# Optimization experiments

Measured on AMD Instinct MI355X. Metric: run time of the kernel, lower is better.

The kernel has to match this reference:

```python
import jax, jax.numpy as jnp
import numpy as np

N = 100000   # nodes
DEG = 4      # fixed out-degree (>2 so every node survives the c>2 mask)
E = N * DEG  # edges
IN = 128
H = 256


def _lin_params(key, fan_out, fan_in, bias=True):
    k1, k2 = jax.random.split(key)
    W = 0.05 * jax.random.normal(k1, (fan_out, fan_in), jnp.float32)
    if bias:
        b = 0.05 * jax.random.normal(k2, (fan_out,), jnp.float32)
        return W, b
    return W


def setup_inputs() -> dict:
    key = jax.random.key(0)
    ks = jax.random.split(key, 12)
    x = jax.random.normal(ks[0], (N, IN), jnp.float32)
    # every node has exactly DEG outgoing edges -> out-degree 4 > 2 for all nodes
    src = jnp.repeat(jnp.arange(N, dtype=jnp.int32), DEG)
    dst = jax.random.randint(ks[1], (E,), 0, N, dtype=jnp.int32)
    edge_index = jnp.stack([src, dst])  # [2, E]
    batch = jnp.zeros((N,), jnp.int32)
    Wr0, br0 = _lin_params(ks[2], H, IN)
    Ws0 = _lin_params(ks[3], H, IN, bias=False)
    Wr1, br1 = _lin_params(ks[4], H, H)
    Ws1 = _lin_params(ks[5], H, H, bias=False)
    Wr2, br2 = _lin_params(ks[6], H, H)
    Ws2 = _lin_params(ks[7], H, H, bias=False)
    Wsp1, bsp1 = _lin_params(ks[8], 1, H)
    Wsp2, bsp2 = _lin_params(ks[9], 1, H)
    Wl, bl = _lin_params(ks[10], 1, 2)
    return dict(x=x, edge_index=edge_index, batch=batch,
                Wr0=Wr0, br0=br0, Ws0=Ws0,
                Wr1=Wr1, br1=br1, Ws1=Ws1,
                Wr2=Wr2, br2=br2, Ws2=Ws2,
                Wsp1=Wsp1, bsp1=bsp1, Wsp2=Wsp2, bsp2=bsp2,
                Wl=Wl, bl=bl)


def reference(x, edge_index, batch, Wr0, br0, Ws0, Wr1, br1, Ws1,
              Wr2, br2, Ws2, Wsp1, bsp1, Wsp2, bsp2, Wl, bl):
    src, dst = edge_index[0], edge_index[1]

    def gconv(h, Wr, br, Ws):
        # PyG GraphConv(aggr='add'): out_i = W_rel @ sum_{j->i} h_j + b + W_root @ h_i
        agg = jax.ops.segment_sum(h[src], dst, num_segments=N)
        return jax.nn.relu(agg @ Wr.T + br + h @ Ws.T)

    h = gconv(x, Wr0, br0, Ws0)
    h = gconv(h, Wr1, br1, Ws1)
    h = gconv(h, Wr2, br2, Ws2)

    # unique(edge_index[0], counts) ; keep source nodes with out-degree > 2
    deg = jax.ops.segment_sum(jnp.ones((E,), h.dtype), src, num_segments=N)
    sel = jnp.nonzero(deg > 2, size=N, fill_value=0)[0]  # all N nodes by construction
    xs = h[sel].reshape(-1, 2 * H)  # pair consecutive nodes
    x1, x2 = xs[:, :H], xs[:, H:]
    out = jnp.concatenate([jax.nn.relu(x1 @ Wsp1.T + bsp1),
                           jax.nn.relu(x2 @ Wsp2.T + bsp2)], axis=1)
    y = jax.nn.sigmoid(out @ Wl.T + bl)  # split=True branch
    return y, xs, x1, x2
```

## Files before the change

### kernel.cpp

```cpp
#include <hip/hip_runtime.h>
#include <hip/hip_bf16.h>
#include <math.h>

#define NNODES 100000
#define NEDGES 400000
#define INDIM  128
#define HDIM   256
#define MAXDEG 32

#define BM 128
#define BN 128
#define BK 64
#define MTILES 782
#define GEMM_BLOCKS 1568

typedef __attribute__((ext_vector_type(8))) short short8;
typedef __attribute__((ext_vector_type(8))) unsigned short ushort8v;
typedef __attribute__((ext_vector_type(4))) float f32x4;

__device__ __forceinline__ float bf2f(unsigned short u) {
    union { unsigned int i; float f; } v; v.i = ((unsigned int)u) << 16; return v.f;
}
__device__ __forceinline__ unsigned short f2bf(float f) {
    union { float f; unsigned int i; } v; v.f = f;
    unsigned int r = v.i + 0x7fffu + ((v.i >> 16) & 1u);
    return (unsigned short)(r >> 16);
}

__device__ __forceinline__ void async_load16(const void* g, void* l) {
    __builtin_amdgcn_global_load_lds(
        (const __attribute__((address_space(1))) unsigned int*)g,
        (__attribute__((address_space(3))) unsigned int*)l,
        16, 0, 0);
}

__global__ void build_elist(const int* __restrict__ ei, int* __restrict__ cnt,
                            int* __restrict__ elist) {
    int e = blockIdx.x * 256 + threadIdx.x;
    if (e < NEDGES) {
        int d = ei[NEDGES + e];
        int s = ei[e];
        int pos = atomicAdd(&cnt[d], 1);
        if (pos < MAXDEG) elist[d * MAXDEG + pos] = s;
    }
}

__global__ void convert_x(const float* __restrict__ x, unsigned short* __restrict__ xb) {
    int i = blockIdx.x * 256 + threadIdx.x;
    const int total = NNODES * INDIM / 4;
    if (i < total) {
        float4 v = ((const float4*)x)[i];
        ushort4 o; o.x = f2bf(v.x); o.y = f2bf(v.y); o.z = f2bf(v.z); o.w = f2bf(v.w);
        ((ushort4*)xb)[i] = o;
    }
}

__global__ void convert_w(const float* __restrict__ Wr, const float* __restrict__ Ws,
                          unsigned short* __restrict__ B, int K) {
    int idx = blockIdx.x * 256 + threadIdx.x;
    int tot = HDIM * 2 * K;
    if (idx < tot) {
        int n = idx / (2 * K);
        int k = idx - n * 2 * K;
        float v = (k < K) ? Wr[n * K + k] : Ws[n * K + (k - K)];
        B[idx] = f2bf(v);
    }
}

__global__ void gather_f32(const float* __restrict__ x, const int* __restrict__ cnt,
                           const int* __restrict__ elist, unsigned short* __restrict__ agg) {
    int wid  = (blockIdx.x * blockDim.x + threadIdx.x) >> 6;
    int lane = threadIdx.x & 63;
    if (wid >= NNODES) return;
    int c = cnt[wid]; if (c > MAXDEG) c = MAXDEG;
    const int4* el4 = (const int4*)(elist + wid * MAXDEG);
    float a0 = 0.f, a1 = 0.f;
    for (int j0 = 0; j0 < c; j0 += 4) {
        int4 e = el4[j0 >> 2];
        int rem = c - j0;
        float2 v0 = {0.f,0.f}, v1 = {0.f,0.f}, v2 = {0.f,0.f}, v3 = {0.f,0.f};
        v0 = ((const float2*)(x + (size_t)e.x * INDIM))[lane];
        if (rem > 1) v1 = ((const float2*)(x + (size_t)e.y * INDIM))[lane];
        if (rem > 2) v2 = ((const float2*)(x + (size_t)e.z * INDIM))[lane];
        if (rem > 3) v3 = ((const float2*)(x + (size_t)e.w * INDIM))[lane];
        a0 += v0.x + v1.x + v2.x + v3.x;
        a1 += v0.y + v1.y + v2.y + v3.y;
    }
    ushort2 o; o.x = f2bf(a0); o.y = f2bf(a1);
    ((ushort2*)(agg + (size_t)wid * INDIM))[lane] = o;
}

__global__ void gather_bf16(const unsigned short* __restrict__ h, const int* __restrict__ cnt,
                            const int* __restrict__ elist, unsigned short* __restrict__ agg) {
    int wid  = (blockIdx.x * blockDim.x + threadIdx.x) >> 6;
    int lane = threadIdx.x & 63;
    if (wid >= NNODES) return;
    int c = cnt[wid]; if (c > MAXDEG) c = MAXDEG;
    const int4* el4 = (const int4*)(elist + wid * MAXDEG);
    float a0 = 0.f, a1 = 0.f, a2 = 0.f, a3 = 0.f;
    for (int j0 = 0; j0 < c; j0 += 4) {
        int4 e = el4[j0 >> 2];
        int rem = c - j0;
        ushort4 v0 = {0,0,0,0}, v1 = {0,0,0,0}, v2 = {0,0,0,0}, v3 = {0,0,0,0};
        v0 = ((const ushort4*)(h + (size_t)e.x * HDIM))[lane];
        if (rem > 1) v1 = ((const ushort4*)(h + (size_t)e.y * HDIM))[lane];
        if (rem > 2) v2 = ((const ushort4*)(h + (size_t)e.z * HDIM))[lane];
        if (rem > 3) v3 = ((const ushort4*)(h + (size_t)e.w * HDIM))[lane];
        a0 += bf2f(v0.x) + bf2f(v1.x) + bf2f(v2.x) + bf2f(v3.x);
        a1 += bf2f(v0.y) + bf2f(v1.y) + bf2f(v2.y) + bf2f(v3.y);
        a2 += bf2f(v0.z) + bf2f(v1.z) + bf2f(v2.z) + bf2f(v3.z);
        a3 += bf2f(v0.w) + bf2f(v1.w) + bf2f(v2.w) + bf2f(v3.w);
    }
    ushort4 o; o.x = f2bf(a0); o.y = f2bf(a1); o.z = f2bf(a2); o.w = f2bf(a3);
    ((ushort4*)(agg + (size_t)wid * HDIM))[lane] = o;
}

template<int MODE>
__global__ __launch_bounds__(256)
void gemm_kernel(const unsigned short* __restrict__ A1, const unsigned short* __restrict__ A2,
                 int K, const unsigned short* __restrict__ B, const float* __restrict__ bias,
                 unsigned short* __restrict__ hout,
                 float* __restrict__ xs, float* __restrict__ x1o, float* __restrict__ x2o,
                 const float* __restrict__ Wsp1, const float* __restrict__ Wsp2,
                 float* __restrict__ spart) {
    __shared__ __align__(16) unsigned char smem[(BM * BK + BN * BK) * 2];
    unsigned short* Ash = (unsigned short*)smem;
    unsigned short* Bsh = Ash + BM * BK;

    int u = blockIdx.x;
    int g = u >> 4, r = u & 15;
    int ny = (r >> 3) & 1;
    int mx = g * 8 + (r & 7);
    if (mx >= MTILES) return;

    const int tid  = threadIdx.x;
    const int lane = tid & 63;
    const int wave = tid >> 6;
    const int wm = wave >> 1, wn = wave & 1;
    const int m0 = mx * BM;
    const int n0 = ny * BN;
    const int Ktot = 2 * K;

    f32x4 acc[4][4];
    for (int i = 0; i < 4; i++)
        for (int j = 0; j < 4; j++)
            acc[i][j] = (f32x4){0.f, 0.f, 0.f, 0.f};

    for (int k0 = 0; k0 < Ktot; k0 += BK) {
        const unsigned short* Abase; int koff;
        if (k0 < K) { Abase = A1; koff = k0; } else { Abase = A2; koff = k0 - K; }

        #pragma unroll
        for (int it = 0; it < 4; it++) {
            int idx = it * 256 + tid;
            int row = idx >> 3, seg = idx & 7;
            int gseg = seg ^ (row & 7);
            int grow = m0 + row; if (grow >= NNODES) grow = NNODES - 1;
            async_load16(Abase + (size_t)grow * K + koff + gseg * 8, &Ash[idx * 8]);
        }
        #pragma unroll
        for (int it = 0; it < 4; it++) {
            int idx = it * 256 + tid;
            int row = idx >> 3, seg = idx & 7;
            int gseg = seg ^ (row & 7);
            int grow = n0 + row;
            async_load16(B + (size_t)grow * Ktot + k0 + gseg * 8, &Bsh[idx * 8]);
        }
        __syncthreads();

        #pragma unroll
        for (int half = 0; half < 2; half++) {
            short8 af[4], bfr[4];
            #pragma unroll
            for (int mt = 0; mt < 4; mt++) {
                int ml  = wm * 64 + mt * 16 + (lane & 15);
                int seg = half * 4 + (lane >> 4);
                int ps  = seg ^ (ml & 7);
                af[mt] = *(const short8*)&Ash[ml * BK + ps * 8];
            }
            #pragma unroll
            for (int nt = 0; nt < 4; nt++) {
                int nl  = wn * 64 + nt * 16 + (lane & 15);
                int seg = half * 4 + (lane >> 4);
                int ps  = seg ^ (nl & 7);
                bfr[nt] = *(const short8*)&Bsh[nl * BK + ps * 8];
            }
            #pragma unroll
            for (int mt = 0; mt < 4; mt++)
                #pragma unroll
                for (int nt = 0; nt < 4; nt++)
                    acc[mt][nt] = __builtin_amdgcn_mfma_f32_16x16x32_bf16(
                        af[mt], bfr[nt], acc[mt][nt], 0, 0, 0);
        }
        __syncthreads();
    }

    float* bounce = (float*)smem;
    float* wb = bounce + wave * (16 * 68);
    const int q    = lane & 3;
    const int rrow = lane >> 2;

    #pragma unroll
    for (int mt = 0; mt < 4; mt++) {
        __syncthreads();
        #pragma unroll
        for (int nt = 0; nt < 4; nt++)
            #pragma unroll
            for (int rr = 0; rr < 4; rr++)
                wb[((lane >> 4) * 4 + rr) * 68 + nt * 16 + (lane & 15)] = acc[mt][nt][rr];
        __syncthreads();

        int grow = m0 + wm * 64 + mt * 16 + rrow;
        int gc   = n0 + wn * 64 + q * 16;
        float4 v[4];
        #pragma unroll
        for (int s = 0; s < 4; s++)
            v[s] = ((const float4*)(wb + rrow * 68 + q * 16))[s];

        if (grow < NNODES) {
            const float4* bv = (const float4*)(bias + gc);
            #pragma unroll
            for (int s = 0; s < 4; s++) {
                float4 b4 = bv[s];
                v[s].x = fmaxf(v[s].x + b4.x, 0.f);
                v[s].y = fmaxf(v[s].y + b4.y, 0.f);
                v[s].z = fmaxf(v[s].z + b4.z, 0.f);
                v[s].w = fmaxf(v[s].w + b4.w, 0.f);
            }
            if (MODE == 0) {
                ushort8v o0, o1;
                o0[0]=f2bf(v[0].x); o0[1]=f2bf(v[0].y); o0[2]=f2bf(v[0].z); o0[3]=f2bf(v[0].w);
                o0[4]=f2bf(v[1].x); o0[5]=f2bf(v[1].y); o0[6]=f2bf(v[1].z); o0[7]=f2bf(v[1].w);
                o1[0]=f2bf(v[2].x); o1[1]=f2bf(v[2].y); o1[2]=f2bf(v[2].z); o1[3]=f2bf(v[2].w);
                o1[4]=f2bf(v[3].x); o1[5]=f2bf(v[3].y); o1[6]=f2bf(v[3].z); o1[7]=f2bf(v[3].w);
                ushort8v* dst = (ushort8v*)(hout + (size_t)grow * HDIM + gc);
                dst[0] = o0; dst[1] = o1;
            } else {
                float4* xsp = (float4*)(xs + (size_t)grow * HDIM + gc);
                #pragma unroll
                for (int s = 0; s < 4; s++) xsp[s] = v[s];
                float* xo = (grow & 1) ? x2o : x1o;
                float4* xop = (float4*)(xo + (size_t)(grow >> 1) * HDIM + gc);
                #pragma unroll
                for (int s = 0; s < 4; s++) xop[s] = v[s];
                const float* wsp = (grow & 1) ? Wsp2 : Wsp1;
                const float4* wv = (const float4*)(wsp + gc);
                float p = 0.f;
                #pragma unroll
                for (int s = 0; s < 4; s++) {
                    float4 w4 = wv[s];
                    p += v[s].x * w4.x + v[s].y * w4.y + v[s].z * w4.z + v[s].w * w4.w;
                }
                p += __shfl_xor(p, 1);
                p += __shfl_xor(p, 2);
                if (q == 0) atomicAdd(&spart[grow], p);
            }
        }
    }
}

__global__ void finalize_kernel(const float* __restrict__ spart, const float* __restrict__ bsp1,
                                const float* __restrict__ bsp2, const float* __restrict__ Wl,
                                const float* __restrict__ bl, float* __restrict__ y) {
    int p = blockIdx.x * 256 + threadIdx.x;
    if (p < NNODES / 2) {
        float s1 = spart[2 * p]     + bsp1[0]; s1 = s1 > 0.f ? s1 : 0.f;
        float s2 = spart[2 * p + 1] + bsp2[0]; s2 = s2 > 0.f ? s2 : 0.f;
        float t = s1 * Wl[0] + s2 * Wl[1] + bl[0];
        y[p] = 1.f / (1.f + expf(-t));
    }
}

extern "C" void kernel_launch(void* const* d_in, const int* in_sizes, int n_in,
                              void* d_out, int out_size, void* d_ws, size_t ws_size,
                              hipStream_t stream) {
    const float* x    = (const float*)d_in[0];
    const int*   ei   = (const int*)d_in[1];
    const float* Wr0  = (const float*)d_in[3];
    const float* br0  = (const float*)d_in[4];
    const float* Ws0  = (const float*)d_in[5];
    const float* Wr1  = (const float*)d_in[6];
    const float* br1  = (const float*)d_in[7];
    const float* Ws1  = (const float*)d_in[8];
    const float* Wr2  = (const float*)d_in[9];
    const float* br2  = (const float*)d_in[10];
    const float* Ws2  = (const float*)d_in[11];
    const float* Wsp1 = (const float*)d_in[12];
    const float* bsp1 = (const float*)d_in[13];
    const float* Wsp2 = (const float*)d_in[14];
    const float* bsp2 = (const float*)d_in[15];
    const float* Wl   = (const float*)d_in[16];
    const float* bl   = (const float*)d_in[17];

    char* ws = (char*)d_ws;
    size_t off = 0;
    auto alloc = [&](size_t bytes) -> void* {
        void* p = ws + off;
        off += (bytes + 255) & ~(size_t)255;
        return p;
    };
    int*            cnt   = (int*)alloc((size_t)NNODES * 4);
    float*          spart = (float*)alloc((size_t)NNODES * 4);
    size_t zero_bytes = off;
    int*            elist = (int*)alloc((size_t)NNODES * MAXDEG * 4);
    unsigned short* xb    = (unsigned short*)alloc((size_t)NNODES * INDIM * 2);
    unsigned short* aggb  = (unsigned short*)alloc((size_t)NNODES * HDIM * 2);
    unsigned short* hA    = (unsigned short*)alloc((size_t)NNODES * HDIM * 2);
    unsigned short* hB    = (unsigned short*)alloc((size_t)NNODES * HDIM * 2);
    unsigned short* B0    = (unsigned short*)alloc((size_t)HDIM * 2 * INDIM * 2);
    unsigned short* B1    = (unsigned short*)alloc((size_t)HDIM * 2 * HDIM * 2);
    unsigned short* B2    = (unsigned short*)alloc((size_t)HDIM * 2 * HDIM * 2);

    float* y  = (float*)d_out;
    float* xs = y + 50000;
    float* x1 = xs + (size_t)50000 * 512;
    float* x2 = x1 + (size_t)50000 * 256;

    hipMemsetAsync(ws, 0, zero_bytes, stream);
    build_elist<<<(NEDGES + 255) / 256, 256, 0, stream>>>(ei, cnt, elist);
    convert_x<<<(NNODES * INDIM / 4 + 255) / 256, 256, 0, stream>>>(x, xb);
    convert_w<<<(HDIM * 2 * INDIM + 255) / 256, 256, 0, stream>>>(Wr0, Ws0, B0, INDIM);
    convert_w<<<(HDIM * 2 * HDIM + 255) / 256, 256, 0, stream>>>(Wr1, Ws1, B1, HDIM);
    convert_w<<<(HDIM * 2 * HDIM + 255) / 256, 256, 0, stream>>>(Wr2, Ws2, B2, HDIM);

    int gather_blocks = (NNODES * 64 + 255) / 256;

    gather_f32<<<gather_blocks, 256, 0, stream>>>(x, cnt, elist, aggb);
    gemm_kernel<0><<<GEMM_BLOCKS, 256, 0, stream>>>(aggb, xb, INDIM, B0, br0, hA,
                                                    nullptr, nullptr, nullptr,
                                                    nullptr, nullptr, nullptr);
    gather_bf16<<<gather_blocks, 256, 0, stream>>>(hA, cnt, elist, aggb);
    gemm_kernel<0><<<GEMM_BLOCKS, 256, 0, stream>>>(aggb, hA, HDIM, B1, br1, hB,
                                                    nullptr, nullptr, nullptr,
                                                    nullptr, nullptr, nullptr);
    gather_bf16<<<gather_blocks, 256, 0, stream>>>(hB, cnt, elist, aggb);
    gemm_kernel<1><<<GEMM_BLOCKS, 256, 0, stream>>>(aggb, hB, HDIM, B2, br2, nullptr,
                                                    xs, x1, x2, Wsp1, Wsp2, spart);
    finalize_kernel<<<(NNODES / 2 + 255) / 256, 256, 0, stream>>>(
        spart, bsp1, bsp2, Wl, bl, y);
}
```

Measured before the change: 618.3 us.

## Use 64x256 GEMM tiles, fuse prep kernels, gather layer-0 from bf16 input

The GEMM tile changes from 128x128 to 64x256. Each block now covers the full output width, so the A rows are read only once, and the wave layout and block indexing are reworked to match. The four prep launches (x conversion, three weight conversions, edge-list build) are merged into one kernel. The first gather now reads the bf16 copy of x instead of fp32, halving the bytes it reads. The trade-off is that each block now loads a larger B tile and layer-0 aggregation sums bf16-rounded inputs.

```diff
diff --git a/kernel.cpp b/kernel.cpp
--- a/kernel.cpp
+++ b/kernel.cpp
@@ -8,11 +8,10 @@
 #define HDIM   256
 #define MAXDEG 32
 
-#define BM 128
-#define BN 128
+#define BM 64
+#define BN 256
 #define BK 64
-#define MTILES 782
-#define GEMM_BLOCKS 1568
+#define MTILES 1563
 
 typedef __attribute__((ext_vector_type(8))) short short8;
 typedef __attribute__((ext_vector_type(8))) unsigned short ushort8v;
@@ -34,9 +33,44 @@
         16, 0, 0);
 }
 
-__global__ void build_elist(const int* __restrict__ ei, int* __restrict__ cnt,
+#define XB_BLOCKS 12500
+#define W0_BLOCKS 256
+#define W1_BLOCKS 512
+#define EL_BLOCKS 1563
+#define PREP_BLOCKS (XB_BLOCKS + W0_BLOCKS + 2 * W1_BLOCKS + EL_BLOCKS)
+
+__global__ void prep_kernel(const float* __restrict__ x, unsigned short* __restrict__ xb,
+                            const float* __restrict__ Wr0, const float* __restrict__ Ws0,
+                            unsigned short* __restrict__ B0,
+                            const float* __restrict__ Wr1, const float* __restrict__ Ws1,
+                            unsigned short* __restrict__ B1,
+                            const float* __restrict__ Wr2, const float* __restrict__ Ws2,
+                            unsigned short* __restrict__ B2,
+                            const int* __restrict__ ei, int* __restrict__ cnt,
                             int* __restrict__ elist) {
-    int e = blockIdx.x * 256 + threadIdx.x;
+    int b = blockIdx.x;
+    if (b < XB_BLOCKS) {
+        int i = b * 256 + threadIdx.x;
+        float4 v = ((const float4*)x)[i];
+        ushort4 o; o.x = f2bf(v.x); o.y = f2bf(v.y); o.z = f2bf(v.z); o.w = f2bf(v.w);
+        ((ushort4*)xb)[i] = o;
+        return;
+    }
+    b -= XB_BLOCKS;
+    if (b < W0_BLOCKS + 2 * W1_BLOCKS) {
+        const float *Wr, *Ws; unsigned short* B; int K;
+        if (b < W0_BLOCKS)               { Wr = Wr0; Ws = Ws0; B = B0; K = INDIM; }
+        else if (b < W0_BLOCKS + W1_BLOCKS) { Wr = Wr1; Ws = Ws1; B = B1; K = HDIM; b -= W0_BLOCKS; }
+        else                              { Wr = Wr2; Ws = Ws2; B = B2; K = HDIM; b -= W0_BLOCKS + W1_BLOCKS; }
+        int idx = b * 256 + threadIdx.x;
+        int n = idx / (2 * K);
+        int k = idx - n * 2 * K;
+        float v = (k < K) ? Wr[n * K + k] : Ws[n * K + (k - K)];
+        B[idx] = f2bf(v);
+        return;
+    }
+    b -= W0_BLOCKS + 2 * W1_BLOCKS;
+    int e = b * 256 + threadIdx.x;
     if (e < NEDGES) {
         int d = ei[NEDGES + e];
         int s = ei[e];
@@ -45,30 +79,8 @@
     }
 }
 
-__global__ void convert_x(const float* __restrict__ x, unsigned short* __restrict__ xb) {
-    int i = blockIdx.x * 256 + threadIdx.x;
-    const int total = NNODES * INDIM / 4;
-    if (i < total) {
-        float4 v = ((const float4*)x)[i];
-        ushort4 o; o.x = f2bf(v.x); o.y = f2bf(v.y); o.z = f2bf(v.z); o.w = f2bf(v.w);
-        ((ushort4*)xb)[i] = o;
-    }
-}
-
-__global__ void convert_w(const float* __restrict__ Wr, const float* __restrict__ Ws,
-                          unsigned short* __restrict__ B, int K) {
-    int idx = blockIdx.x * 256 + threadIdx.x;
-    int tot = HDIM * 2 * K;
-    if (idx < tot) {
-        int n = idx / (2 * K);
-        int k = idx - n * 2 * K;
-        float v = (k < K) ? Wr[n * K + k] : Ws[n * K + (k - K)];
-        B[idx] = f2bf(v);
-    }
-}
-
-__global__ void gather_f32(const float* __restrict__ x, const int* __restrict__ cnt,
-                           const int* __restrict__ elist, unsigned short* __restrict__ agg) {
+__global__ void gather_bf16_128(const unsigned short* __restrict__ h, const int* __restrict__ cnt,
+                                const int* __restrict__ elist, unsigned short* __restrict__ agg) {
     int wid  = (blockIdx.x * blockDim.x + threadIdx.x) >> 6;
     int lane = threadIdx.x & 63;
     if (wid >= NNODES) return;
@@ -78,20 +90,20 @@
     for (int j0 = 0; j0 < c; j0 += 4) {
         int4 e = el4[j0 >> 2];
         int rem = c - j0;
-        float2 v0 = {0.f,0.f}, v1 = {0.f,0.f}, v2 = {0.f,0.f}, v3 = {0.f,0.f};
-        v0 = ((const float2*)(x + (size_t)e.x * INDIM))[lane];
-        if (rem > 1) v1 = ((const float2*)(x + (size_t)e.y * INDIM))[lane];
-        if (rem > 2) v2 = ((const float2*)(x + (size_t)e.z * INDIM))[lane];
-        if (rem > 3) v3 = ((const float2*)(x + (size_t)e.w * INDIM))[lane];
-        a0 += v0.x + v1.x + v2.x + v3.x;
-        a1 += v0.y + v1.y + v2.y + v3.y;
+        ushort2 v0 = {0,0}, v1 = {0,0}, v2 = {0,0}, v3 = {0,0};
+        v0 = ((const ushort2*)(h + (size_t)e.x * INDIM))[lane];
+        if (rem > 1) v1 = ((const ushort2*)(h + (size_t)e.y * INDIM))[lane];
+        if (rem > 2) v2 = ((const ushort2*)(h + (size_t)e.z * INDIM))[lane];
+        if (rem > 3) v3 = ((const ushort2*)(h + (size_t)e.w * INDIM))[lane];
+        a0 += bf2f(v0.x) + bf2f(v1.x) + bf2f(v2.x) + bf2f(v3.x);
+        a1 += bf2f(v0.y) + bf2f(v1.y) + bf2f(v2.y) + bf2f(v3.y);
     }
     ushort2 o; o.x = f2bf(a0); o.y = f2bf(a1);
     ((ushort2*)(agg + (size_t)wid * INDIM))[lane] = o;
 }
 
-__global__ void gather_bf16(const unsigned short* __restrict__ h, const int* __restrict__ cnt,
-                            const int* __restrict__ elist, unsigned short* __restrict__ agg) {
+__global__ void gather_bf16_256(const unsigned short* __restrict__ h, const int* __restrict__ cnt,
+                                const int* __restrict__ elist, unsigned short* __restrict__ agg) {
     int wid  = (blockIdx.x * blockDim.x + threadIdx.x) >> 6;
     int lane = threadIdx.x & 63;
     if (wid >= NNODES) return;
@@ -127,18 +139,10 @@
     unsigned short* Ash = (unsigned short*)smem;
     unsigned short* Bsh = Ash + BM * BK;
 
-    int u = blockIdx.x;
-    int g = u >> 4, r = u & 15;
-    int ny = (r >> 3) & 1;
-    int mx = g * 8 + (r & 7);
-    if (mx >= MTILES) return;
-
     const int tid  = threadIdx.x;
     const int lane = tid & 63;
-    const int wave = tid >> 6;
-    const int wm = wave >> 1, wn = wave & 1;
-    const int m0 = mx * BM;
-    const int n0 = ny * BN;
+    const int wn   = tid >> 6;
+    const int m0   = blockIdx.x * BM;
     const int Ktot = 2 * K;
 
     f32x4 acc[4][4];
@@ -151,7 +155,7 @@
         if (k0 < K) { Abase = A1; koff = k0; } else { Abase = A2; koff = k0 - K; }
 
         #pragma unroll
-        for (int it = 0; it < 4; it++) {
+        for (int it = 0; it < 2; it++) {
             int idx = it * 256 + tid;
             int row = idx >> 3, seg = idx & 7;
             int gseg = seg ^ (row & 7);
@@ -159,12 +163,11 @@
             async_load16(Abase + (size_t)grow * K + koff + gseg * 8, &Ash[idx * 8]);
         }
         #pragma unroll
-        for (int it = 0; it < 4; it++) {
+        for (int it = 0; it < 8; it++) {
             int idx = it * 256 + tid;
             int row = idx >> 3, seg = idx & 7;
             int gseg = seg ^ (row & 7);
-            int grow = n0 + row;
-            async_load16(B + (size_t)grow * Ktot + k0 + gseg * 8, &Bsh[idx * 8]);
+            async_load16(B + (size_t)row * Ktot + k0 + gseg * 8, &Bsh[idx * 8]);
         }
         __syncthreads();
 
@@ -173,7 +176,7 @@
             short8 af[4], bfr[4];
             #pragma unroll
             for (int mt = 0; mt < 4; mt++) {
-                int ml  = wm * 64 + mt * 16 + (lane & 15);
+                int ml  = mt * 16 + (lane & 15);
                 int seg = half * 4 + (lane >> 4);
                 int ps  = seg ^ (ml & 7);
                 af[mt] = *(const short8*)&Ash[ml * BK + ps * 8];
@@ -196,7 +199,7 @@
     }
 
     float* bounce = (float*)smem;
-    float* wb = bounce + wave * (16 * 68);
+    float* wb = bounce + wn * (16 * 68);
     const int q    = lane & 3;
     const int rrow = lane >> 2;
 
@@ -210,8 +213,8 @@
                 wb[((lane >> 4) * 4 + rr) * 68 + nt * 16 + (lane & 15)] = acc[mt][nt][rr];
         __syncthreads();
 
-        int grow = m0 + wm * 64 + mt * 16 + rrow;
-        int gc   = n0 + wn * 64 + q * 16;
+        int grow = m0 + mt * 16 + rrow;
+        int gc   = wn * 64 + q * 16;
         float4 v[4];
         #pragma unroll
         for (int s = 0; s < 4; s++)
@@ -317,25 +320,22 @@
     float* x2 = x1 + (size_t)50000 * 256;
 
     hipMemsetAsync(ws, 0, zero_bytes, stream);
-    build_elist<<<(NEDGES + 255) / 256, 256, 0, stream>>>(ei, cnt, elist);
-    convert_x<<<(NNODES * INDIM / 4 + 255) / 256, 256, 0, stream>>>(x, xb);
-    convert_w<<<(HDIM * 2 * INDIM + 255) / 256, 256, 0, stream>>>(Wr0, Ws0, B0, INDIM);
-    convert_w<<<(HDIM * 2 * HDIM + 255) / 256, 256, 0, stream>>>(Wr1, Ws1, B1, HDIM);
-    convert_w<<<(HDIM * 2 * HDIM + 255) / 256, 256, 0, stream>>>(Wr2, Ws2, B2, HDIM);
+    prep_kernel<<<PREP_BLOCKS, 256, 0, stream>>>(x, xb, Wr0, Ws0, B0, Wr1, Ws1, B1,
+                                                 Wr2, Ws2, B2, ei, cnt, elist);
 
     int gather_blocks = (NNODES * 64 + 255) / 256;
 
-    gather_f32<<<gather_blocks, 256, 0, stream>>>(x, cnt, elist, aggb);
-    gemm_kernel<0><<<GEMM_BLOCKS, 256, 0, stream>>>(aggb, xb, INDIM, B0, br0, hA,
-                                                    nullptr, nullptr, nullptr,
-                                                    nullptr, nullptr, nullptr);
-    gather_bf16<<<gather_blocks, 256, 0, stream>>>(hA, cnt, elist, aggb);
-    gemm_kernel<0><<<GEMM_BLOCKS, 256, 0, stream>>>(aggb, hA, HDIM, B1, br1, hB,
-                                                    nullptr, nullptr, nullptr,
-                                                    nullptr, nullptr, nullptr);
-    gather_bf16<<<gather_blocks, 256, 0, stream>>>(hB, cnt, elist, aggb);
-    gemm_kernel<1><<<GEMM_BLOCKS, 256, 0, stream>>>(aggb, hB, HDIM, B2, br2, nullptr,
-                                                    xs, x1, x2, Wsp1, Wsp2, spart);
+    gather_bf16_128<<<gather_blocks, 256, 0, stream>>>(xb, cnt, elist, aggb);
+    gemm_kernel<0><<<MTILES, 256, 0, stream>>>(aggb, xb, INDIM, B0, br0, hA,
+                                               nullptr, nullptr, nullptr,
+                                               nullptr, nullptr, nullptr);
+    gather_bf16_256<<<gather_blocks, 256, 0, stream>>>(hA, cnt, elist, aggb);
+    gemm_kernel<0><<<MTILES, 256, 0, stream>>>(aggb, hA, HDIM, B1, br1, hB,
+                                               nullptr, nullptr, nullptr,
+                                               nullptr, nullptr, nullptr);
+    gather_bf16_256<<<gather_blocks, 256, 0, stream>>>(hB, cnt, elist, aggb);
+    gemm_kernel<1><<<MTILES, 256, 0, stream>>>(aggb, hB, HDIM, B2, br2, nullptr,
+                                               xs, x1, x2, Wsp1, Wsp2, spart);
     finalize_kernel<<<(NNODES / 2 + 255) / 256, 256, 0, stream>>>(
         spart, bsp1, bsp2, Wl, bl, y);
 }
```

Result: no change. 607.1 us (-1.8%).
